# Kernel tuning notes

Hardware: AMD Instinct MI355X
Metric: run time of the kernel (lower is better)

## Reference

```python
import jax, jax.numpy as jnp
import numpy as np

CLASS_WEIGHTS = np.array([0.03203128, 0.12453853, 0.12360233, 0.12430233, 0.1118631,
                          0.11928928, 0.12498565, 0.12078846, 0.11859904], dtype=np.float32)


def setup_inputs() -> dict:
    key = jax.random.key(0)
    k1, k2 = jax.random.split(key)
    N, C = 4_000_000, 9
    logits = jax.random.normal(k1, (N, C), dtype=jnp.float32)
    target = jax.random.randint(k2, (N,), 0, C, dtype=jnp.int64)
    class_weights = jnp.asarray(CLASS_WEIGHTS)
    return {"logits": logits, "target": target, "class_weights": class_weights}


def reference(logits, target, class_weights):
    # log_softmax over class dim (dim=1 for 2D input, matching nn.LogSoftmax legacy default)
    log_probs = jax.nn.log_softmax(logits, axis=-1)  # [N, C]
    # Faithful but efficient form of log_probs.index_select(-1, target).diag():
    # direct per-row gather of the target-class log-prob, O(N) not O(N^2).
    lp_target = jnp.take_along_axis(log_probs, target[:, None], axis=-1)[:, 0]  # [N]
    losses = -class_weights[target] * lp_target  # [N]
    # size_average=True, batch_all=True branch -> tuple
    nonzero = (losses > 1e-16).sum().astype(jnp.float32)
    loss_nonzero_mean = losses.sum() / (nonzero + 1e-16)
    return (loss_nonzero_mean, losses.mean())
```

## Files before the change

### kernel.cpp

```cpp
#include <hip/hip_runtime.h>

#define THREADS 256
#define MAX_GRID 2048

typedef float f4 __attribute__((ext_vector_type(4)));
struct f4u { f4 v; } __attribute__((packed, aligned(4)));

__global__ __launch_bounds__(THREADS) void ce_main_kernel(
    const float* __restrict__ logits,
    const int*   __restrict__ target,
    const float* __restrict__ cw,
    float2*      __restrict__ partials,
    int N)
{
    __shared__ float rsum[THREADS / 64];
    __shared__ float rcnt[THREADS / 64];

    const int t      = threadIdx.x;
    const int tid    = blockIdx.x * THREADS + t;
    const int stride = gridDim.x * THREADS;

    float lsum = 0.0f;
    float lcnt = 0.0f;

    for (int r = tid; r < N; r += stride) {
        const int tg = target[r];
        const float* __restrict__ row = logits + (size_t)r * 9;
        const f4u* p = (const f4u*)row;
        const f4 a = p[0].v;
        const f4 b = p[1].v;
        const float c = row[8];
        const float xt = row[tg];
        const float w  = cw[tg];

        float m = fmaxf(fmaxf(fmaxf(a.x, a.y), fmaxf(a.z, a.w)),
                        fmaxf(fmaxf(b.x, b.y), fmaxf(b.z, b.w)));
        m = fmaxf(m, c);
        float s = __expf(a.x - m) + __expf(a.y - m) + __expf(a.z - m) + __expf(a.w - m)
                + __expf(b.x - m) + __expf(b.y - m) + __expf(b.z - m) + __expf(b.w - m)
                + __expf(c - m);
        const float loss = -w * (xt - m - __logf(s));
        lsum += loss;
        lcnt += (loss > 1e-16f) ? 1.0f : 0.0f;
    }

    #pragma unroll
    for (int off = 32; off > 0; off >>= 1) {
        lsum += __shfl_down(lsum, off);
        lcnt += __shfl_down(lcnt, off);
    }
    const int wave = t >> 6;
    if ((t & 63) == 0) { rsum[wave] = lsum; rcnt[wave] = lcnt; }
    __syncthreads();
    if (t == 0) {
        float bs = 0.0f, bc = 0.0f;
        #pragma unroll
        for (int w2 = 0; w2 < THREADS / 64; ++w2) { bs += rsum[w2]; bc += rcnt[w2]; }
        partials[blockIdx.x] = make_float2(bs, bc);
    }
}

__global__ __launch_bounds__(THREADS) void ce_finalize_kernel(
    const float2* __restrict__ partials, float* __restrict__ out,
    int nPartials, float invN)
{
    __shared__ float rsum[THREADS / 64];
    __shared__ float rcnt[THREADS / 64];
    const int t = threadIdx.x;
    float s = 0.0f, c = 0.0f;
    for (int i = t; i < nPartials; i += THREADS) {
        const float2 p = partials[i];
        s += p.x; c += p.y;
    }
    #pragma unroll
    for (int off = 32; off > 0; off >>= 1) {
        s += __shfl_down(s, off);
        c += __shfl_down(c, off);
    }
    const int wave = t >> 6;
    if ((t & 63) == 0) { rsum[wave] = s; rcnt[wave] = c; }
    __syncthreads();
    if (t == 0) {
        float S = 0.0f, C = 0.0f;
        #pragma unroll
        for (int w2 = 0; w2 < THREADS / 64; ++w2) { S += rsum[w2]; C += rcnt[w2]; }
        out[0] = S / (C + 1e-16f);
        out[1] = S * invN;
    }
}

extern "C" void kernel_launch(void* const* d_in, const int* in_sizes, int n_in,
                              void* d_out, int out_size, void* d_ws, size_t ws_size,
                              hipStream_t stream) {
    const float* logits = (const float*)d_in[0];
    const int*   target = (const int*)d_in[1];
    const float* cw     = (const float*)d_in[2];
    float* out = (float*)d_out;
    float2* partials = (float2*)d_ws;

    const int N = in_sizes[1];

    int grid = MAX_GRID;
    const int maxByWs = (int)(ws_size / sizeof(float2));
    if (grid > maxByWs) grid = maxByWs;
    const int maxByN = (N + THREADS - 1) / THREADS;
    if (grid > maxByN) grid = maxByN;

    ce_main_kernel<<<grid, THREADS, 0, stream>>>(logits, target, cw, partials, N);
    ce_finalize_kernel<<<1, THREADS, 0, stream>>>(partials, out, grid, 1.0f / (float)N);
}
```

Measured before the change: 216.2 us.

## Process four rows per thread with aligned 16-byte vector loads

Each thread now handles four consecutive rows (36 floats), loaded as nine aligned float4 vectors, plus one int4 load for the four targets. This replaces the grid-stride loop and its unaligned packed-float4 row reads. The grid is now sized to cover N with one pass instead of a fixed 2048 blocks. Because there is no longer a loop, rows beyond the grid would be skipped if the workspace cap ever limits the grid below what N requires.

```diff
diff --git a/kernel.cpp b/kernel.cpp
--- a/kernel.cpp
+++ b/kernel.cpp
@@ -1,10 +1,24 @@
 #include <hip/hip_runtime.h>
 
 #define THREADS 256
-#define MAX_GRID 2048
 
 typedef float f4 __attribute__((ext_vector_type(4)));
-struct f4u { f4 v; } __attribute__((packed, aligned(4)));
+
+__device__ __forceinline__ void row9(
+    float e0, float e1, float e2, float e3, float e4,
+    float e5, float e6, float e7, float e8,
+    float xt, float w, float& lsum, float& lcnt)
+{
+    float m = fmaxf(fmaxf(fmaxf(e0, e1), fmaxf(e2, e3)),
+                    fmaxf(fmaxf(e4, e5), fmaxf(e6, e7)));
+    m = fmaxf(m, e8);
+    float s = __expf(e0 - m) + __expf(e1 - m) + __expf(e2 - m) + __expf(e3 - m)
+            + __expf(e4 - m) + __expf(e5 - m) + __expf(e6 - m) + __expf(e7 - m)
+            + __expf(e8 - m);
+    const float loss = -w * (xt - m - __logf(s));
+    lsum += loss;
+    lcnt += (loss > 1e-16f) ? 1.0f : 0.0f;
+}
 
 __global__ __launch_bounds__(THREADS) void ce_main_kernel(
     const float* __restrict__ logits,
@@ -16,32 +30,35 @@
     __shared__ float rsum[THREADS / 64];
     __shared__ float rcnt[THREADS / 64];
 
-    const int t      = threadIdx.x;
-    const int tid    = blockIdx.x * THREADS + t;
-    const int stride = gridDim.x * THREADS;
+    const int tid = blockIdx.x * THREADS + threadIdx.x;
+    const int r0  = tid * 4;
 
-    float lsum = 0.0f;
-    float lcnt = 0.0f;
+    float lsum = 0.0f, lcnt = 0.0f;
 
-    for (int r = tid; r < N; r += stride) {
-        const int tg = target[r];
-        const float* __restrict__ row = logits + (size_t)r * 9;
-        const f4u* p = (const f4u*)row;
-        const f4 a = p[0].v;
-        const f4 b = p[1].v;
-        const float c = row[8];
-        const float xt = row[tg];
-        const float w  = cw[tg];
+    if (r0 + 3 < N) {
+        const int4 tg = *(const int4*)(target + r0);
+        const f4* __restrict__ p = (const f4*)(logits + (size_t)r0 * 9);
+        const f4 v0 = p[0], v1 = p[1], v2 = p[2], v3 = p[3], v4 = p[4],
+                 v5 = p[5], v6 = p[6], v7 = p[7], v8 = p[8];
 
-        float m = fmaxf(fmaxf(fmaxf(a.x, a.y), fmaxf(a.z, a.w)),
-                        fmaxf(fmaxf(b.x, b.y), fmaxf(b.z, b.w)));
-        m = fmaxf(m, c);
-        float s = __expf(a.x - m) + __expf(a.y - m) + __expf(a.z - m) + __expf(a.w - m)
-                + __expf(b.x - m) + __expf(b.y - m) + __expf(b.z - m) + __expf(b.w - m)
-                + __expf(c - m);
-        const float loss = -w * (xt - m - __logf(s));
-        lsum += loss;
-        lcnt += (loss > 1e-16f) ? 1.0f : 0.0f;
+        const float* __restrict__ row = logits + (size_t)r0 * 9;
+        const float xt0 = row[tg.x];
+        const float xt1 = row[9  + tg.y];
+        const float xt2 = row[18 + tg.z];
+        const float xt3 = row[27 + tg.w];
+        const float w0 = cw[tg.x], w1 = cw[tg.y], w2 = cw[tg.z], w3 = cw[tg.w];
+
+        row9(v0.x, v0.y, v0.z, v0.w, v1.x, v1.y, v1.z, v1.w, v2.x, xt0, w0, lsum, lcnt);
+        row9(v2.y, v2.z, v2.w, v3.x, v3.y, v3.z, v3.w, v4.x, v4.y, xt1, w1, lsum, lcnt);
+        row9(v4.z, v4.w, v5.x, v5.y, v5.z, v5.w, v6.x, v6.y, v6.z, xt2, w2, lsum, lcnt);
+        row9(v6.w, v7.x, v7.y, v7.z, v7.w, v8.x, v8.y, v8.z, v8.w, xt3, w3, lsum, lcnt);
+    } else if (r0 < N) {
+        for (int r = r0; r < N && r < r0 + 4; ++r) {
+            const float* __restrict__ x = logits + (size_t)r * 9;
+            const int t = target[r];
+            row9(x[0], x[1], x[2], x[3], x[4], x[5], x[6], x[7], x[8],
+                 x[t], cw[t], lsum, lcnt);
+        }
     }
 
     #pragma unroll
@@ -49,10 +66,10 @@
         lsum += __shfl_down(lsum, off);
         lcnt += __shfl_down(lcnt, off);
     }
-    const int wave = t >> 6;
-    if ((t & 63) == 0) { rsum[wave] = lsum; rcnt[wave] = lcnt; }
+    const int wave = threadIdx.x >> 6;
+    if ((threadIdx.x & 63) == 0) { rsum[wave] = lsum; rcnt[wave] = lcnt; }
     __syncthreads();
-    if (t == 0) {
+    if (threadIdx.x == 0) {
         float bs = 0.0f, bc = 0.0f;
         #pragma unroll
         for (int w2 = 0; w2 < THREADS / 64; ++w2) { bs += rsum[w2]; bc += rcnt[w2]; }
@@ -99,12 +116,10 @@
     float2* partials = (float2*)d_ws;
 
     const int N = in_sizes[1];
-
-    int grid = MAX_GRID;
+    const int nThreadsNeeded = (N + 3) / 4;
+    int grid = (nThreadsNeeded + THREADS - 1) / THREADS;
     const int maxByWs = (int)(ws_size / sizeof(float2));
     if (grid > maxByWs) grid = maxByWs;
-    const int maxByN = (N + THREADS - 1) / THREADS;
-    if (grid > maxByN) grid = maxByN;
 
     ce_main_kernel<<<grid, THREADS, 0, stream>>>(logits, target, cw, partials, N);
     ce_finalize_kernel<<<1, THREADS, 0, stream>>>(partials, out, grid, 1.0f / (float)N);
```

Result: slower. 220.9 us (+2.2%).

## Stage logits through LDS with coalesced wave loads, one row per thread

Applied to the files above, without the earlier changes.

Each wave now loads its 64 rows of logits as contiguous float4 chunks, which gives coalesced global reads, and stages them in shared memory before each thread reads its own 9-element row. The grid-stride loop is replaced by one row per thread across a much larger grid, and the max subtraction in log-softmax is dropped. Class weights are also cached in LDS, and the finalize kernel uses 1024 threads to reduce the larger partials array. Risks: without the max shift, large logits can overflow exp. If the workspace caps the grid, rows beyond the cap are never processed. The 9-float row stride in LDS may cause bank conflicts.

```diff
diff --git a/kernel.cpp b/kernel.cpp
--- a/kernel.cpp
+++ b/kernel.cpp
@@ -1,47 +1,65 @@
 #include <hip/hip_runtime.h>
 
 #define THREADS 256
-#define MAX_GRID 2048
+#define WAVES 4
+#define SLAB 592
+#define FIN_THREADS 1024
 
 typedef float f4 __attribute__((ext_vector_type(4)));
-struct f4u { f4 v; } __attribute__((packed, aligned(4)));
 
-__global__ __launch_bounds__(THREADS) void ce_main_kernel(
+__global__ __launch_bounds__(THREADS, 8) void ce_main_kernel(
     const float* __restrict__ logits,
     const int*   __restrict__ target,
     const float* __restrict__ cw,
     float2*      __restrict__ partials,
     int N)
 {
-    __shared__ float rsum[THREADS / 64];
-    __shared__ float rcnt[THREADS / 64];
+    __shared__ float slab[WAVES * SLAB];
+    __shared__ float rs[WAVES], rc[WAVES];
 
-    const int t      = threadIdx.x;
-    const int tid    = blockIdx.x * THREADS + t;
-    const int stride = gridDim.x * THREADS;
+    const int t    = threadIdx.x;
+    const int wave = t >> 6;
+    const int lane = t & 63;
+    const int blockRow0 = blockIdx.x * (WAVES * 64);
+    const int row0 = blockRow0 + wave * 64;
+    const int row  = row0 + lane;
 
-    float lsum = 0.0f;
-    float lcnt = 0.0f;
+    float lsum = 0.0f, lcnt = 0.0f;
 
-    for (int r = tid; r < N; r += stride) {
-        const int tg = target[r];
-        const float* __restrict__ row = logits + (size_t)r * 9;
-        const f4u* p = (const f4u*)row;
-        const f4 a = p[0].v;
-        const f4 b = p[1].v;
-        const float c = row[8];
-        const float xt = row[tg];
-        const float w  = cw[tg];
+    if (blockRow0 + WAVES * 64 <= N) {
+        float* sl = slab + wave * SLAB;
+        const float* base = logits + (size_t)row0 * 9;
 
-        float m = fmaxf(fmaxf(fmaxf(a.x, a.y), fmaxf(a.z, a.w)),
-                        fmaxf(fmaxf(b.x, b.y), fmaxf(b.z, b.w)));
-        m = fmaxf(m, c);
-        float s = __expf(a.x - m) + __expf(a.y - m) + __expf(a.z - m) + __expf(a.w - m)
-                + __expf(b.x - m) + __expf(b.y - m) + __expf(b.z - m) + __expf(b.w - m)
-                + __expf(c - m);
-        const float loss = -w * (xt - m - __logf(s));
-        lsum += loss;
-        lcnt += (loss > 1e-16f) ? 1.0f : 0.0f;
+        const f4   cA = *(const f4*)(base + 4 * lane);
+        const f4   cB = *(const f4*)(base + 256 + 4 * lane);
+        const float cC = base[512 + lane];
+        const int   tg = target[row];
+
+        if (lane < 9) sl[576 + lane] = cw[lane];
+
+        *(f4*)(sl + 4 * lane) = cA;
+        *(f4*)(sl + 256 + 4 * lane) = cB;
+        sl[512 + lane] = cC;
+        __syncthreads();
+
+        const float* x = sl + 9 * lane;
+        float s = __expf(x[0]) + __expf(x[1]) + __expf(x[2]) + __expf(x[3])
+                + __expf(x[4]) + __expf(x[5]) + __expf(x[6]) + __expf(x[7])
+                + __expf(x[8]);
+        const float xt = x[tg];
+        const float w  = sl[576 + tg];
+        const float loss = w * (__logf(s) - xt);
+        lsum = loss;
+        lcnt = (loss > 1e-16f) ? 1.0f : 0.0f;
+    } else if (row < N) {
+        const float* x = logits + (size_t)row * 9;
+        const int tg = target[row];
+        float s = 0.0f;
+        #pragma unroll
+        for (int c = 0; c < 9; ++c) s += __expf(x[c]);
+        const float loss = cw[tg] * (__logf(s) - x[tg]);
+        lsum = loss;
+        lcnt = (loss > 1e-16f) ? 1.0f : 0.0f;
     }
 
     #pragma unroll
@@ -49,26 +67,24 @@
         lsum += __shfl_down(lsum, off);
         lcnt += __shfl_down(lcnt, off);
     }
-    const int wave = t >> 6;
-    if ((t & 63) == 0) { rsum[wave] = lsum; rcnt[wave] = lcnt; }
+    if (lane == 0) { rs[wave] = lsum; rc[wave] = lcnt; }
     __syncthreads();
     if (t == 0) {
         float bs = 0.0f, bc = 0.0f;
         #pragma unroll
-        for (int w2 = 0; w2 < THREADS / 64; ++w2) { bs += rsum[w2]; bc += rcnt[w2]; }
+        for (int v = 0; v < WAVES; ++v) { bs += rs[v]; bc += rc[v]; }
         partials[blockIdx.x] = make_float2(bs, bc);
     }
 }
 
-__global__ __launch_bounds__(THREADS) void ce_finalize_kernel(
+__global__ __launch_bounds__(FIN_THREADS) void ce_finalize_kernel(
     const float2* __restrict__ partials, float* __restrict__ out,
     int nPartials, float invN)
 {
-    __shared__ float rsum[THREADS / 64];
-    __shared__ float rcnt[THREADS / 64];
+    __shared__ float rs[FIN_THREADS / 64], rc[FIN_THREADS / 64];
     const int t = threadIdx.x;
     float s = 0.0f, c = 0.0f;
-    for (int i = t; i < nPartials; i += THREADS) {
+    for (int i = t; i < nPartials; i += FIN_THREADS) {
         const float2 p = partials[i];
         s += p.x; c += p.y;
     }
@@ -78,12 +94,12 @@
         c += __shfl_down(c, off);
     }
     const int wave = t >> 6;
-    if ((t & 63) == 0) { rsum[wave] = s; rcnt[wave] = c; }
+    if ((t & 63) == 0) { rs[wave] = s; rc[wave] = c; }
     __syncthreads();
     if (t == 0) {
         float S = 0.0f, C = 0.0f;
         #pragma unroll
-        for (int w2 = 0; w2 < THREADS / 64; ++w2) { S += rsum[w2]; C += rcnt[w2]; }
+        for (int v = 0; v < FIN_THREADS / 64; ++v) { S += rs[v]; C += rc[v]; }
         out[0] = S / (C + 1e-16f);
         out[1] = S * invN;
     }
@@ -99,13 +115,10 @@
     float2* partials = (float2*)d_ws;
 
     const int N = in_sizes[1];
-
-    int grid = MAX_GRID;
+    int grid = (N + THREADS - 1) / THREADS;
     const int maxByWs = (int)(ws_size / sizeof(float2));
     if (grid > maxByWs) grid = maxByWs;
-    const int maxByN = (N + THREADS - 1) / THREADS;
-    if (grid > maxByN) grid = maxByN;
 
     ce_main_kernel<<<grid, THREADS, 0, stream>>>(logits, target, cw, partials, N);
-    ce_finalize_kernel<<<1, THREADS, 0, stream>>>(partials, out, grid, 1.0f / (float)N);
+    ce_finalize_kernel<<<1, FIN_THREADS, 0, stream>>>(partials, out, grid, 1.0f / (float)N);
 }
```

Result: no change. 217.0 us (+0.4%).
